# Kernel optimization log

Hardware: AMD Instinct MI355X
Metric: run time of the kernel (lower is better)

Reference implementation:

```python
import jax, jax.numpy as jnp
import numpy as np

N_BASIS = 7      # n_weights_per_edge
DEGREE = 3       # cubic B-splines
LO, HI = -1.0, 1.0
# clamped/open-uniform knot vector of length N_BASIS + DEGREE + 1 = 11
_KNOTS = np.concatenate([np.full(DEGREE, LO), np.linspace(LO, HI, N_BASIS - DEGREE + 1), np.full(DEGREE, HI)]).astype(np.float32)


def bspline_basis(x):
    """Cox-de Boor cubic B-spline basis. x: [...] -> [..., N_BASIS]."""
    t = jnp.asarray(_KNOTS, dtype=x.dtype)
    xe = jnp.clip(x, LO, HI - 1e-6)[..., None]
    N = ((xe >= t[:-1]) & (xe < t[1:])).astype(x.dtype)  # [..., 10]
    for d in range(1, DEGREE + 1):
        ld = t[d:-1] - t[:-(d + 1)]
        rd = t[d + 1:] - t[1:-d]
        left = jnp.where(ld > 0, (xe - t[:-(d + 1)]) / jnp.where(ld > 0, ld, 1.0), 0.0) * N[..., :-1]
        right = jnp.where(rd > 0, (t[d + 1:] - xe) / jnp.where(rd > 0, rd, 1.0), 0.0) * N[..., 1:]
        N = left + right
    return N  # [..., 7]


def extract_patches(x, k=3):
    # x [B,C,H,W] -> [B,Ho,Wo,C*k*k], channel-major flatten matching region.flatten()
    B, C, H, W = x.shape
    Ho, Wo = H - k + 1, W - k + 1
    cols = [x[:, :, i:i + Ho, j:j + Wo] for i in range(k) for j in range(k)]  # k*k x [B,C,Ho,Wo]
    p = jnp.stack(cols, axis=2).reshape(B, C * k * k, Ho, Wo)
    return jnp.transpose(p, (0, 2, 3, 1))


def kan_conv(x, W):
    # W: [out_ch, C*k*k, N_BASIS]; out[b,o,i,j] = sum_e sum_k W[o,e,k]*B_k(patch[b,i,j,e])
    patches = extract_patches(x, 3)               # [B,Ho,Wo,E]
    bases = bspline_basis(patches)                 # [B,Ho,Wo,E,7]
    return jnp.einsum('bhwek,oek->bohw', bases, W)


def kan_dense(v, W):
    # v: [n_in], W: [n_out, n_in, 7]
    bases = bspline_basis(v)                       # [n_in,7]
    return jnp.einsum('ek,oek->o', bases, W)


def setup_inputs() -> dict:
    key = jax.random.key(0)
    k0, k1, k2, k3, k4 = jax.random.split(key, 5)
    H = W = 384
    n_in = (H - 4) * (W - 4)  # 144400
    u = lambda k, s: jax.random.uniform(k, s, jnp.float32, -1.0, 1.0)  # weights_range=[-1,1]
    return {
        'x': jax.random.normal(k0, (1, 3, H, W), jnp.float32),
        'W1': u(k1, (2, 3 * 9, N_BASIS)),
        'W2': u(k2, (1, 2 * 9, N_BASIS)),
        'W3': u(k3, (32, n_in, N_BASIS)),
        'W4': u(k4, (10, 32, N_BASIS)),
    }


def reference(x, W1, W2, W3, W4):
    h = kan_conv(x, W1)     # [1,2,382,382]
    h = kan_conv(h, W2)     # [1,1,380,380]
    v = h.reshape(-1)       # flatten (batch==1)
    h1 = kan_dense(v, W3)   # [32]
    out = kan_dense(h1, W4) # [10]
    return out
```

## Files before the change

### kernel.cpp

```cpp
#include <hip/hip_runtime.h>

typedef float f32x4 __attribute__((ext_vector_type(4)));

__device__ __forceinline__ void bspline7(float x, float B[7]) {
    constexpr float t[11] = {-1.f, -1.f, -1.f, -1.f, -0.5f, 0.f, 0.5f, 1.f, 1.f, 1.f, 1.f};
    float xe = fminf(fmaxf(x, -1.f), 0.999999f);
    float N[10];
#pragma unroll
    for (int i = 0; i < 10; ++i)
        N[i] = (xe >= t[i] && xe < t[i + 1]) ? 1.f : 0.f;
#pragma unroll
    for (int d = 1; d <= 3; ++d) {
#pragma unroll
        for (int i = 0; i + d < 10; ++i) {
            float ld = t[i + d] - t[i];
            float rd = t[i + d + 1] - t[i + 1];
            float left  = (ld > 0.f) ? (xe - t[i]) / ld * N[i] : 0.f;
            float right = (rd > 0.f) ? (t[i + d + 1] - xe) / rd * N[i + 1] : 0.f;
            N[i] = left + right;
        }
    }
#pragma unroll
    for (int k = 0; k < 7; ++k) B[k] = N[k];
}

#define H0 384
#define H1 382
#define H2 380
#define NP2 (H2 * H2)
#define L_DENSE (NP2 * 7)
#define L4_DENSE (L_DENSE / 4)
#define TILE 16
#define HTILE 18
#define XTILE 20

__global__ __launch_bounds__(256) void k_fused(const float* __restrict__ x,
                                               const float* __restrict__ W1,
                                               const float* __restrict__ W2,
                                               float* __restrict__ Bv,
                                               float* __restrict__ acc32) {
    __shared__ float w1[378];
    __shared__ float w2[126];
    __shared__ float bx[3 * XTILE * XTILE * 7];
    __shared__ float bh[2 * HTILE * HTILE * 7];

    const int tid = threadIdx.x;
    const int i0 = blockIdx.y * TILE;
    const int j0 = blockIdx.x * TILE;

    if (blockIdx.x == 0 && blockIdx.y == 0 && tid < 32) acc32[tid] = 0.f;

    for (int i = tid; i < 378; i += 256) w1[i] = W1[i];
    for (int i = tid; i < 126; i += 256) w2[i] = W2[i];

    for (int t = tid; t < 3 * XTILE * XTILE; t += 256) {
        int c = t / (XTILE * XTILE);
        int r = t % (XTILE * XTILE);
        int ii = r / XTILE, jj = r % XTILE;
        int gi = i0 + ii, gj = j0 + jj;
        float xv = (gi < H0 && gj < H0) ? x[(c * H0 + gi) * H0 + gj] : 0.f;
        float B[7];
        bspline7(xv, B);
#pragma unroll
        for (int k = 0; k < 7; ++k) bx[t * 7 + k] = B[k];
    }
    __syncthreads();

    for (int t = tid; t < HTILE * HTILE; t += 256) {
        int i1 = t / HTILE, j1 = t % HTILE;
        float acc0 = 0.f, acc1 = 0.f;
#pragma unroll
        for (int c = 0; c < 3; ++c)
#pragma unroll
            for (int di = 0; di < 3; ++di)
#pragma unroll
                for (int dj = 0; dj < 3; ++dj) {
                    const float* b = &bx[(((c * XTILE) + (i1 + di)) * XTILE + (j1 + dj)) * 7];
                    int e = c * 9 + di * 3 + dj;
                    const float* u0 = &w1[e * 7];
                    const float* u1 = &w1[189 + e * 7];
#pragma unroll
                    for (int k = 0; k < 7; ++k) {
                        float bvv = b[k];
                        acc0 += bvv * u0[k];
                        acc1 += bvv * u1[k];
                    }
                }
        float B0[7], B1[7];
        bspline7(acc0, B0);
        bspline7(acc1, B1);
#pragma unroll
        for (int k = 0; k < 7; ++k) {
            bh[t * 7 + k] = B0[k];
            bh[(HTILE * HTILE + t) * 7 + k] = B1[k];
        }
    }
    __syncthreads();

    int li = tid / TILE, lj = tid % TILE;
    int gi2 = i0 + li, gj2 = j0 + lj;
    if (gi2 < H2 && gj2 < H2) {
        float acc = 0.f;
#pragma unroll
        for (int c = 0; c < 2; ++c)
#pragma unroll
            for (int di = 0; di < 3; ++di)
#pragma unroll
                for (int dj = 0; dj < 3; ++dj) {
                    const float* b = &bh[((c * HTILE + (li + di)) * HTILE + (lj + dj)) * 7];
                    const float* u = &w2[(c * 9 + di * 3 + dj) * 7];
#pragma unroll
                    for (int k = 0; k < 7; ++k) acc += b[k] * u[k];
                }
        float B[7];
        bspline7(acc, B);
        size_t p = (size_t)gi2 * H2 + gj2;
#pragma unroll
        for (int k = 0; k < 7; ++k) Bv[p * 7 + k] = B[k];
    }
}

__global__ __launch_bounds__(256) void k_dense1(const float* __restrict__ W3,
                                                const float* __restrict__ Bv,
                                                float* __restrict__ acc32) {
    int o = blockIdx.y;
    const f32x4* w = (const f32x4*)(W3 + (size_t)o * L_DENSE);
    const f32x4* b = (const f32x4*)Bv;
    float s = 0.f;
    for (int f = blockIdx.x * blockDim.x + threadIdx.x; f < L4_DENSE;
         f += gridDim.x * blockDim.x) {
        f32x4 wv = __builtin_nontemporal_load(&w[f]);
        f32x4 bv = b[f];
        s += wv.x * bv.x + wv.y * bv.y + wv.z * bv.z + wv.w * bv.w;
    }
#pragma unroll
    for (int off = 32; off > 0; off >>= 1) s += __shfl_down(s, off, 64);
    __shared__ float red[4];
    if ((threadIdx.x & 63) == 0) red[threadIdx.x >> 6] = s;
    __syncthreads();
    if (threadIdx.x == 0)
        atomicAdd(&acc32[o], red[0] + red[1] + red[2] + red[3]);
}

__global__ void k_dense2(const float* __restrict__ acc32, const float* __restrict__ W4,
                         float* __restrict__ out) {
    int o = threadIdx.x;
    if (o >= 10) return;
    float s = 0.f;
    for (int e = 0; e < 32; ++e) {
        float B[7];
        bspline7(acc32[e], B);
#pragma unroll
        for (int k = 0; k < 7; ++k) s += B[k] * W4[(o * 32 + e) * 7 + k];
    }
    out[o] = s;
}

extern "C" void kernel_launch(void* const* d_in, const int* in_sizes, int n_in,
                              void* d_out, int out_size, void* d_ws, size_t ws_size,
                              hipStream_t stream) {
    const float* x  = (const float*)d_in[0];
    const float* W1 = (const float*)d_in[1];
    const float* W2 = (const float*)d_in[2];
    const float* W3 = (const float*)d_in[3];
    const float* W4 = (const float*)d_in[4];
    float* out = (float*)d_out;

    char* ws = (char*)d_ws;
    float* acc32 = (float*)ws;
    float* Bv = (float*)(ws + 128);

    dim3 gfuse((H2 + TILE - 1) / TILE, (H2 + TILE - 1) / TILE);
    k_fused<<<gfuse, 256, 0, stream>>>(x, W1, W2, Bv, acc32);
    k_dense1<<<dim3(64, 32), 256, 0, stream>>>(W3, Bv, acc32);
    k_dense2<<<1, 64, 0, stream>>>(acc32, W4, out);
}
```

Measured before the change: 258.1 us.

## Compute all 32 dense outputs per thread to reuse basis vector loads

The first dense layer kernel now has each thread handle all 32 output rows for its slice of the basis vector. Each basis element is loaded once and reused against 32 weight rows, instead of being re-read once per output across a 2D grid. This cuts basis-vector traffic, but it adds 32 accumulator registers, 32 wavefront reductions at the end, and a 1D grid of 512 blocks. The nontemporal hint on the weight loads is dropped, and the basis buffer offset in the workspace is moved.

```diff
diff --git a/kernel.cpp b/kernel.cpp
--- a/kernel.cpp
+++ b/kernel.cpp
@@ -33,6 +33,7 @@
 #define TILE 16
 #define HTILE 18
 #define XTILE 20
+#define D1_GRID 512
 
 __global__ __launch_bounds__(256) void k_fused(const float* __restrict__ x,
                                                const float* __restrict__ W1,
@@ -123,23 +124,38 @@
 __global__ __launch_bounds__(256) void k_dense1(const float* __restrict__ W3,
                                                 const float* __restrict__ Bv,
                                                 float* __restrict__ acc32) {
-    int o = blockIdx.y;
-    const f32x4* w = (const f32x4*)(W3 + (size_t)o * L_DENSE);
-    const f32x4* b = (const f32x4*)Bv;
-    float s = 0.f;
-    for (int f = blockIdx.x * blockDim.x + threadIdx.x; f < L4_DENSE;
-         f += gridDim.x * blockDim.x) {
-        f32x4 wv = __builtin_nontemporal_load(&w[f]);
-        f32x4 bv = b[f];
-        s += wv.x * bv.x + wv.y * bv.y + wv.z * bv.z + wv.w * bv.w;
+    const f32x4* __restrict__ w4 = (const f32x4*)W3;
+    const f32x4* __restrict__ b4 = (const f32x4*)Bv;
+
+    float s[32];
+#pragma unroll
+    for (int o = 0; o < 32; ++o) s[o] = 0.f;
+
+    for (int f = blockIdx.x * 256 + threadIdx.x; f < L4_DENSE; f += D1_GRID * 256) {
+        f32x4 bv = b4[f];
+#pragma unroll
+        for (int o = 0; o < 32; ++o) {
+            f32x4 wv = w4[(size_t)o * L4_DENSE + f];
+            s[o] += wv.x * bv.x + wv.y * bv.y + wv.z * bv.z + wv.w * bv.w;
+        }
     }
+
+    __shared__ float red[4][32];
+    const int lane = threadIdx.x & 63;
+    const int wid = threadIdx.x >> 6;
 #pragma unroll
-    for (int off = 32; off > 0; off >>= 1) s += __shfl_down(s, off, 64);
-    __shared__ float red[4];
-    if ((threadIdx.x & 63) == 0) red[threadIdx.x >> 6] = s;
+    for (int o = 0; o < 32; ++o) {
+        float v = s[o];
+#pragma unroll
+        for (int off = 32; off > 0; off >>= 1) v += __shfl_down(v, off, 64);
+        if (lane == 0) red[wid][o] = v;
+    }
     __syncthreads();
-    if (threadIdx.x == 0)
-        atomicAdd(&acc32[o], red[0] + red[1] + red[2] + red[3]);
+    if (threadIdx.x < 32) {
+        int o = threadIdx.x;
+        float v = red[0][o] + red[1][o] + red[2][o] + red[3][o];
+        atomicAdd(&acc32[o], v);
+    }
 }
 
 __global__ void k_dense2(const float* __restrict__ acc32, const float* __restrict__ W4,
@@ -168,10 +184,10 @@
 
     char* ws = (char*)d_ws;
     float* acc32 = (float*)ws;
-    float* Bv = (float*)(ws + 128);
+    float* Bv = (float*)(ws + 256);
 
     dim3 gfuse((H2 + TILE - 1) / TILE, (H2 + TILE - 1) / TILE);
     k_fused<<<gfuse, 256, 0, stream>>>(x, W1, W2, Bv, acc32);
-    k_dense1<<<dim3(64, 32), 256, 0, stream>>>(W3, Bv, acc32);
+    k_dense1<<<D1_GRID, 256, 0, stream>>>(W3, Bv, acc32);
     k_dense2<<<1, 64, 0, stream>>>(acc32, W4, out);
 }
```

New measurement: 263.5 us. +2.1%, slower.
